# Kernel optimization log

Hardware: AMD Instinct MI355X
Metric: run time of the kernel (lower is better)

Reference implementation:

```python
import jax, jax.numpy as jnp
import numpy as np


def setup_inputs() -> dict:
    key = jax.random.key(0)
    k1, k2, k3 = jax.random.split(key, 3)
    B, D = 4096, 512
    out_ftir = jax.random.normal(k1, (B, D), dtype=jnp.float32)
    out_raman = jax.random.normal(k2, (B, D), dtype=jnp.float32)
    labels = jax.random.randint(k3, (B,), 0, 1000, dtype=jnp.int64)
    # learned parameter: log_tau = log(1/init_tau), init_tau = 0.07
    log_tau = jnp.asarray(np.log(1.0 / 0.07), dtype=jnp.float32)
    return {"out_ftir": out_ftir, "out_raman": out_raman, "labels": labels, "log_tau": log_tau}


def reference(out_ftir, out_raman, labels, log_tau):
    # temperature scale, clamped above at 100
    tau = jnp.minimum(jnp.exp(log_tau), 100.0)
    # [B, B] similarity logits
    logits = (out_ftir @ out_raman.T) * tau
    # CLIP-style symmetric cross-entropy with diagonal targets (arange(B)).
    # Note: original torch code's loop over positive off-diagonal pairs
    # computes an unused tensor and does not affect the output.
    raman_lp = jnp.diagonal(jax.nn.log_softmax(logits, axis=-1))   # rows: ftir -> raman
    ftir_lp = jnp.diagonal(jax.nn.log_softmax(logits.T, axis=-1))  # cols: raman -> ftir
    raman_loss = -jnp.mean(raman_lp)
    ftir_loss = -jnp.mean(ftir_lp)
    return (ftir_loss + raman_loss) / 2.0
```

## Files before the change

kernel.cpp:

```cpp
#include <hip/hip_runtime.h>
#include <hip/hip_bf16.h>
#include <stdint.h>


typedef float f32x4 __attribute__((ext_vector_type(4)));
typedef __bf16 bf16x8 __attribute__((ext_vector_type(8)));
typedef __bf16 bf16x4 __attribute__((ext_vector_type(4)));

#define B_DIM 4096
#define D_DIM 512
#define NCHUNK 32

__device__ __forceinline__ void gld_lds16(const void* g, void* l) {
  __builtin_amdgcn_global_load_lds(
      (const __attribute__((address_space(1))) unsigned int*)g,
      (__attribute__((address_space(3))) unsigned int*)l,
      16, 0, 0);
}

__global__ __launch_bounds__(256) void cast_diag_kernel(
    const float* __restrict__ A, const float* __restrict__ Bm,
    __bf16* __restrict__ Abf, __bf16* __restrict__ Bbf,
    float* __restrict__ diagp, float* __restrict__ acc,
    unsigned* __restrict__ counter) {
  if (blockIdx.x == 0 && threadIdx.x == 0) { acc[0] = 0.f; counter[0] = 0u; }
  const float4* A4 = (const float4*)A;
  const float4* B4 = (const float4*)Bm;
  bf16x4* Ab4 = (bf16x4*)Abf;
  bf16x4* Bb4 = (bf16x4*)Bbf;
  int idx = blockIdx.x * 256 + threadIdx.x;
  float local = 0.f;
  #pragma unroll
  for (int it = 0; it < 4; ++it, idx += 512 * 256) {
    int row = idx >> 7, el4 = idx & 127;
    int g = (el4 >> 1) & 3;
    int gswz = g ^ ((row >> 1) & 3);
    int el4p = (el4 & ~6) | (gswz << 1);
    int pidx = row * 128 + el4p;
    float4 va = A4[idx], vb = B4[idx];
    bf16x4 oa, ob;
    oa[0] = (__bf16)va.x; oa[1] = (__bf16)va.y; oa[2] = (__bf16)va.z; oa[3] = (__bf16)va.w;
    ob[0] = (__bf16)vb.x; ob[1] = (__bf16)vb.y; ob[2] = (__bf16)vb.z; ob[3] = (__bf16)vb.w;
    Ab4[pidx] = oa; Bb4[pidx] = ob;
    local += va.x*vb.x + va.y*vb.y + va.z*vb.z + va.w*vb.w;
  }
  #pragma unroll
  for (int off = 1; off < 64; off <<= 1) local += __shfl_xor(local, off);
  __shared__ float red[4];
  int w = threadIdx.x >> 6, lane = threadIdx.x & 63;
  if (lane == 0) red[w] = local;
  __syncthreads();
  if (threadIdx.x == 0)
    diagp[blockIdx.x] = red[0] + red[1] + red[2] + red[3];
}

__global__ __launch_bounds__(256, 3) void gemm_lse_kernel(
    const __bf16* __restrict__ A, const __bf16* __restrict__ Bm,
    const float* __restrict__ log_tau,
    float* __restrict__ row_pmax, float* __restrict__ row_psum,
    float* __restrict__ col_pmax, float* __restrict__ col_psum) {
  __shared__ char smem[49152];
  const int blk = blockIdx.x;
  const int xcd = blk & 7, loc = blk >> 3;
  const int bm = (xcd & 3) * 8 + (loc & 7);
  const int bn = (xcd >> 2) * 16 + (loc >> 3);
  const int t = threadIdx.x;
  const int lane = t & 63;
  const int w = t >> 6;
  const int wm = (w >> 1) * 64, wn = (w & 1) * 64;
  const int q = lane >> 4, c16 = lane & 15;
  const int kbs = q ^ ((c16 >> 1) & 3);

  f32x4 acc[4][4] = {};

  const char* Ag = (const char*)A + (size_t)(bm * 128 + (t >> 2)) * 1024 + (t & 3) * 16;
  const char* Bg = (const char*)Bm + (size_t)(bn * 128 + (t >> 2)) * 1024 + (t & 3) * 16;

  #define ISSUE_STAGE(kt, p)                                                  \
    do {                                                                      \
      const char* ag = Ag + (kt) * 64;                                        \
      const char* bg = Bg + (kt) * 64;                                        \
      char* Al = smem + (p) * 16384 + t * 16;                                 \
      char* Bl = smem + (p) * 16384 + 8192 + t * 16;                          \
      _Pragma("unroll")                                                       \
      for (int i = 0; i < 2; ++i) {                                           \
        gld_lds16(ag + i * 65536, Al + i * 4096);                             \
        gld_lds16(bg + i * 65536, Bl + i * 4096);                             \
      }                                                                       \
    } while (0)

  #define COMPUTE(p)                                                          \
    do {                                                                      \
      const char* Ab = smem + (p) * 16384;                                    \
      const char* Bb = Ab + 8192;                                             \
      bf16x8 af[4], bfr[4];                                                   \
      _Pragma("unroll")                                                       \
      for (int mi = 0; mi < 4; ++mi)                                          \
        af[mi] = *(const bf16x8*)(Ab + (wm + mi * 16 + c16) * 64 + kbs * 16); \
      _Pragma("unroll")                                                       \
      for (int ni = 0; ni < 4; ++ni)                                          \
        bfr[ni] = *(const bf16x8*)(Bb + (wn + ni * 16 + c16) * 64 + kbs * 16);\
      _Pragma("unroll")                                                       \
      for (int mi = 0; mi < 4; ++mi)                                          \
        _Pragma("unroll")                                                     \
        for (int ni = 0; ni < 4; ++ni)                                        \
          acc[mi][ni] = __builtin_amdgcn_mfma_f32_16x16x32_bf16(              \
              af[mi], bfr[ni], acc[mi][ni], 0, 0, 0);                         \
    } while (0)

  ISSUE_STAGE(0, 0);
  ISSUE_STAGE(1, 1);
  for (int kt = 0; kt < 15; ++kt) {
    asm volatile("s_waitcnt vmcnt(4)" ::: "memory");
    __builtin_amdgcn_s_barrier();
    asm volatile("" ::: "memory");
    if (kt < 14) ISSUE_STAGE(kt + 2, (kt + 2) % 3);
    COMPUTE(kt % 3);
  }
  asm volatile("s_waitcnt vmcnt(0)" ::: "memory");
  __builtin_amdgcn_s_barrier();
  asm volatile("" ::: "memory");
  COMPUTE(15 % 3);
  __syncthreads();
  #undef ISSUE_STAGE
  #undef COMPUTE

  const float tau = fminf(__expf(log_tau[0]), 100.0f);
  #pragma unroll
  for (int mi = 0; mi < 4; ++mi)
    #pragma unroll
    for (int ni = 0; ni < 4; ++ni)
      acc[mi][ni] *= tau;

  float2* rbuf = (float2*)smem;
  #pragma unroll
  for (int mi = 0; mi < 4; ++mi)
    #pragma unroll
    for (int r = 0; r < 4; ++r) {
      float v0 = acc[mi][0][r], v1 = acc[mi][1][r], v2 = acc[mi][2][r], v3 = acc[mi][3][r];
      float m = fmaxf(fmaxf(v0, v1), fmaxf(v2, v3));
      float s = __expf(v0 - m) + __expf(v1 - m) + __expf(v2 - m) + __expf(v3 - m);
      int R = wm + mi * 16 + q * 4 + r;
      rbuf[R * 33 + (w & 1) * 16 + c16] = make_float2(m, s);
    }
  __syncthreads();
  if (t < 128) {
    float M = rbuf[t * 33].x;
    #pragma unroll
    for (int x = 1; x < 32; ++x) M = fmaxf(M, rbuf[t * 33 + x].x);
    float S = 0.f;
    #pragma unroll
    for (int x = 0; x < 32; ++x) { float2 p = rbuf[t * 33 + x]; S += p.y * __expf(p.x - M); }
    row_pmax[bn * B_DIM + bm * 128 + t] = M;
    row_psum[bn * B_DIM + bm * 128 + t] = S;
  }
  __syncthreads();
  float2* cbuf = (float2*)smem;
  #pragma unroll
  for (int ni = 0; ni < 4; ++ni) {
    float m = -3.0e38f;
    #pragma unroll
    for (int mi = 0; mi < 4; ++mi)
      #pragma unroll
      for (int r = 0; r < 4; ++r) m = fmaxf(m, acc[mi][ni][r]);
    float s = 0.f;
    #pragma unroll
    for (int mi = 0; mi < 4; ++mi)
      #pragma unroll
      for (int r = 0; r < 4; ++r) s += __expf(acc[mi][ni][r] - m);
    int C = wn + ni * 16 + c16;
    cbuf[C * 9 + (w >> 1) * 4 + q] = make_float2(m, s);
  }
  __syncthreads();
  if (t < 128) {
    float M = cbuf[t * 9].x;
    #pragma unroll
    for (int y = 1; y < 8; ++y) M = fmaxf(M, cbuf[t * 9 + y].x);
    float S = 0.f;
    #pragma unroll
    for (int y = 0; y < 8; ++y) { float2 p = cbuf[t * 9 + y]; S += p.y * __expf(p.x - M); }
    col_pmax[bm * B_DIM + bn * 128 + t] = M;
    col_psum[bm * B_DIM + bn * 128 + t] = S;
  }
}

__global__ __launch_bounds__(256) void combine_kernel(
    const float* __restrict__ row_pmax, const float* __restrict__ row_psum,
    const float* __restrict__ col_pmax, const float* __restrict__ col_psum,
    const float* __restrict__ diagp, const float* __restrict__ log_tau,
    float* __restrict__ acc, unsigned* __restrict__ counter,
    float* __restrict__ out) {
  const int t = threadIdx.x;
  const int item = blockIdx.x * 256 + t;
  const float* pm; const float* ps; int i;
  if (item < B_DIM) { pm = row_pmax; ps = row_psum; i = item; }
  else              { pm = col_pmax; ps = col_psum; i = item - B_DIM; }
  float M = pm[i];
  #pragma unroll
  for (int k = 1; k < NCHUNK; ++k) M = fmaxf(M, pm[k * B_DIM + i]);
  float S = 0.f;
  #pragma unroll
  for (int k = 0; k < NCHUNK; ++k) S += ps[k * B_DIM + i] * __expf(pm[k * B_DIM + i] - M);
  float local = M + __logf(S);
  if (blockIdx.x == 0) {
    float tau = fminf(__expf(log_tau[0]), 100.0f);
    local += -2.0f * tau * (diagp[t] + diagp[t + 256]);
  }
  #pragma unroll
  for (int off = 1; off < 64; off <<= 1) local += __shfl_xor(local, off);
  __shared__ float red[4];
  int w = t >> 6, lane = t & 63;
  if (lane == 0) red[w] = local;
  __syncthreads();
  if (t == 0) {
    atomicAdd(acc, red[0] + red[1] + red[2] + red[3]);
    __threadfence();
    unsigned old = atomicAdd(counter, 1u);
    if (old == 31u) {
      float v = atomicAdd(acc, 0.0f);
      out[0] = v * (1.0f / 8192.0f);
    }
  }
}

extern "C" void kernel_launch(void* const* d_in, const int* in_sizes, int n_in,
                              void* d_out, int out_size, void* d_ws, size_t ws_size,
                              hipStream_t stream) {
  const float* ftir    = (const float*)d_in[0];
  const float* raman   = (const float*)d_in[1];
  const float* log_tau = (const float*)d_in[3];
  float* out = (float*)d_out;

  char* ws = (char*)d_ws;
  __bf16* Abf     = (__bf16*)(ws);
  __bf16* Bbf     = (__bf16*)(ws + (4u << 20));
  float* row_pmax = (float*)(ws + (8u << 20));
  float* row_psum = (float*)(ws + (8u << 20) + (512u << 10));
  float* col_pmax = (float*)(ws + (9u << 20));
  float* col_psum = (float*)(ws + (9u << 20) + (512u << 10));
  float* diagp    = (float*)(ws + (10u << 20));
  float* acc      = (float*)(ws + (10u << 20) + 4096);
  unsigned* cnt   = (unsigned*)(ws + (10u << 20) + 4096 + 4);

  cast_diag_kernel<<<512, 256, 0, stream>>>(ftir, raman, Abf, Bbf, diagp, acc, cnt);
  gemm_lse_kernel<<<1024, 256, 0, stream>>>(Abf, Bbf, log_tau,
                                            row_pmax, row_psum, col_pmax, col_psum);
  combine_kernel<<<32, 256, 0, stream>>>(row_pmax, row_psum, col_pmax, col_psum,
                                         diagp, log_tau, acc, cnt, out);
}
```

Measured before the change: 96.82 us.

## Fuse fp32-to-bf16 cast and diagonal into GEMM via register-staged loads

Removes the separate cast/diagonal kernel. The GEMM now loads fp32 inputs straight into registers, converts them to bf16 and writes swizzled tiles to LDS in a two-stage register-prefetch pipeline, in place of the earlier three-stage direct global-to-LDS async loads. The diagonal term is taken from the MFMA accumulators of the diagonal tiles and added atomically. This saves one launch and the bf16 round trip through global memory, but the GEMM now reads twice as many bytes and does the conversion in its main loop with a shallower pipeline, and the diagonal now comes from bf16 products rather than fp32.

```diff
diff --git a/kernel.cpp b/kernel.cpp
--- a/kernel.cpp
+++ b/kernel.cpp
@@ -5,61 +5,18 @@
 
 typedef float f32x4 __attribute__((ext_vector_type(4)));
 typedef __bf16 bf16x8 __attribute__((ext_vector_type(8)));
-typedef __bf16 bf16x4 __attribute__((ext_vector_type(4)));
 
 #define B_DIM 4096
 #define D_DIM 512
 #define NCHUNK 32
 
-__device__ __forceinline__ void gld_lds16(const void* g, void* l) {
-  __builtin_amdgcn_global_load_lds(
-      (const __attribute__((address_space(1))) unsigned int*)g,
-      (__attribute__((address_space(3))) unsigned int*)l,
-      16, 0, 0);
-}
-
-__global__ __launch_bounds__(256) void cast_diag_kernel(
-    const float* __restrict__ A, const float* __restrict__ Bm,
-    __bf16* __restrict__ Abf, __bf16* __restrict__ Bbf,
-    float* __restrict__ diagp, float* __restrict__ acc,
-    unsigned* __restrict__ counter) {
-  if (blockIdx.x == 0 && threadIdx.x == 0) { acc[0] = 0.f; counter[0] = 0u; }
-  const float4* A4 = (const float4*)A;
-  const float4* B4 = (const float4*)Bm;
-  bf16x4* Ab4 = (bf16x4*)Abf;
-  bf16x4* Bb4 = (bf16x4*)Bbf;
-  int idx = blockIdx.x * 256 + threadIdx.x;
-  float local = 0.f;
-  #pragma unroll
-  for (int it = 0; it < 4; ++it, idx += 512 * 256) {
-    int row = idx >> 7, el4 = idx & 127;
-    int g = (el4 >> 1) & 3;
-    int gswz = g ^ ((row >> 1) & 3);
-    int el4p = (el4 & ~6) | (gswz << 1);
-    int pidx = row * 128 + el4p;
-    float4 va = A4[idx], vb = B4[idx];
-    bf16x4 oa, ob;
-    oa[0] = (__bf16)va.x; oa[1] = (__bf16)va.y; oa[2] = (__bf16)va.z; oa[3] = (__bf16)va.w;
-    ob[0] = (__bf16)vb.x; ob[1] = (__bf16)vb.y; ob[2] = (__bf16)vb.z; ob[3] = (__bf16)vb.w;
-    Ab4[pidx] = oa; Bb4[pidx] = ob;
-    local += va.x*vb.x + va.y*vb.y + va.z*vb.z + va.w*vb.w;
-  }
-  #pragma unroll
-  for (int off = 1; off < 64; off <<= 1) local += __shfl_xor(local, off);
-  __shared__ float red[4];
-  int w = threadIdx.x >> 6, lane = threadIdx.x & 63;
-  if (lane == 0) red[w] = local;
-  __syncthreads();
-  if (threadIdx.x == 0)
-    diagp[blockIdx.x] = red[0] + red[1] + red[2] + red[3];
-}
-
 __global__ __launch_bounds__(256, 3) void gemm_lse_kernel(
-    const __bf16* __restrict__ A, const __bf16* __restrict__ Bm,
+    const float* __restrict__ Af, const float* __restrict__ Bf,
     const float* __restrict__ log_tau,
     float* __restrict__ row_pmax, float* __restrict__ row_psum,
-    float* __restrict__ col_pmax, float* __restrict__ col_psum) {
-  __shared__ char smem[49152];
+    float* __restrict__ col_pmax, float* __restrict__ col_psum,
+    float* __restrict__ accg) {
+  __shared__ char smem[34816];
   const int blk = blockIdx.x;
   const int xcd = blk & 7, loc = blk >> 3;
   const int bm = (xcd & 3) * 8 + (loc & 7);
@@ -73,20 +30,39 @@
 
   f32x4 acc[4][4] = {};
 
-  const char* Ag = (const char*)A + (size_t)(bm * 128 + (t >> 2)) * 1024 + (t & 3) * 16;
-  const char* Bg = (const char*)Bm + (size_t)(bn * 128 + (t >> 2)) * 1024 + (t & 3) * 16;
-
-  #define ISSUE_STAGE(kt, p)                                                  \
+  const int srow = t >> 1;
+  const int sw   = (t >> 2) & 3;
+  const int kb0  = (t & 1) * 2;
+  const float4* Ag0 = (const float4*)(Af + (size_t)(bm * 128 + srow) * D_DIM) + (t & 1) * 4;
+  const float4* Bg0 = (const float4*)(Bf + (size_t)(bn * 128 + srow) * D_DIM) + (t & 1) * 4;
+  const int ldsA = srow * 64 ;
+
+  float4 a0, a1, a2, a3, b0, b1, b2, b3;
+
+  #define LOADS(kt)                                                           \
     do {                                                                      \
-      const char* ag = Ag + (kt) * 64;                                        \
-      const char* bg = Bg + (kt) * 64;                                        \
-      char* Al = smem + (p) * 16384 + t * 16;                                 \
-      char* Bl = smem + (p) * 16384 + 8192 + t * 16;                          \
-      _Pragma("unroll")                                                       \
-      for (int i = 0; i < 2; ++i) {                                           \
-        gld_lds16(ag + i * 65536, Al + i * 4096);                             \
-        gld_lds16(bg + i * 65536, Bl + i * 4096);                             \
-      }                                                                       \
+      const float4* ag = Ag0 + (kt) * 8;                                      \
+      const float4* bg = Bg0 + (kt) * 8;                                      \
+      a0 = ag[0]; a1 = ag[1]; a2 = ag[2]; a3 = ag[3];                         \
+      b0 = bg[0]; b1 = bg[1]; b2 = bg[2]; b3 = bg[3];                         \
+    } while (0)
+
+  #define COMMIT(p)                                                           \
+    do {                                                                      \
+      bf16x8 pa0, pa1, pb0, pb1;                                              \
+      pa0[0]=(__bf16)a0.x; pa0[1]=(__bf16)a0.y; pa0[2]=(__bf16)a0.z; pa0[3]=(__bf16)a0.w; \
+      pa0[4]=(__bf16)a1.x; pa0[5]=(__bf16)a1.y; pa0[6]=(__bf16)a1.z; pa0[7]=(__bf16)a1.w; \
+      pa1[0]=(__bf16)a2.x; pa1[1]=(__bf16)a2.y; pa1[2]=(__bf16)a2.z; pa1[3]=(__bf16)a2.w; \
+      pa1[4]=(__bf16)a3.x; pa1[5]=(__bf16)a3.y; pa1[6]=(__bf16)a3.z; pa1[7]=(__bf16)a3.w; \
+      pb0[0]=(__bf16)b0.x; pb0[1]=(__bf16)b0.y; pb0[2]=(__bf16)b0.z; pb0[3]=(__bf16)b0.w; \
+      pb0[4]=(__bf16)b1.x; pb0[5]=(__bf16)b1.y; pb0[6]=(__bf16)b1.z; pb0[7]=(__bf16)b1.w; \
+      pb1[0]=(__bf16)b2.x; pb1[1]=(__bf16)b2.y; pb1[2]=(__bf16)b2.z; pb1[3]=(__bf16)b2.w; \
+      pb1[4]=(__bf16)b3.x; pb1[5]=(__bf16)b3.y; pb1[6]=(__bf16)b3.z; pb1[7]=(__bf16)b3.w; \
+      char* base = smem + (p) * 16384;                                        \
+      *(bf16x8*)(base + ldsA + ((kb0 ^ sw)) * 16)        = pa0;               \
+      *(bf16x8*)(base + ldsA + (((kb0 + 1) ^ sw)) * 16)  = pa1;               \
+      *(bf16x8*)(base + 8192 + ldsA + ((kb0 ^ sw)) * 16)       = pb0;         \
+      *(bf16x8*)(base + 8192 + ldsA + (((kb0 + 1) ^ sw)) * 16) = pb1;         \
     } while (0)
 
   #define COMPUTE(p)                                                          \
@@ -108,21 +84,17 @@
               af[mi], bfr[ni], acc[mi][ni], 0, 0, 0);                         \
     } while (0)
 
-  ISSUE_STAGE(0, 0);
-  ISSUE_STAGE(1, 1);
-  for (int kt = 0; kt < 15; ++kt) {
-    asm volatile("s_waitcnt vmcnt(4)" ::: "memory");
-    __builtin_amdgcn_s_barrier();
-    asm volatile("" ::: "memory");
-    if (kt < 14) ISSUE_STAGE(kt + 2, (kt + 2) % 3);
-    COMPUTE(kt % 3);
-  }
-  asm volatile("s_waitcnt vmcnt(0)" ::: "memory");
-  __builtin_amdgcn_s_barrier();
-  asm volatile("" ::: "memory");
-  COMPUTE(15 % 3);
-  __syncthreads();
-  #undef ISSUE_STAGE
+  LOADS(0);
+  COMMIT(0);
+  for (int kt = 0; kt < 16; ++kt) {
+    __syncthreads();
+    if (kt < 15) LOADS(kt + 1);
+    COMPUTE(kt & 1);
+    if (kt < 15) COMMIT((kt + 1) & 1);
+  }
+  __syncthreads();
+  #undef LOADS
+  #undef COMMIT
   #undef COMPUTE
 
   const float tau = fminf(__expf(log_tau[0]), 100.0f);
@@ -131,6 +103,20 @@
     #pragma unroll
     for (int ni = 0; ni < 4; ++ni)
       acc[mi][ni] *= tau;
+
+  if (bm == bn && (w == 0 || w == 3)) {
+    float dsum = 0.f;
+    int r = c16 - (q << 2);
+    #pragma unroll
+    for (int rr = 0; rr < 4; ++rr)
+      if (rr == r) {
+        #pragma unroll
+        for (int mi = 0; mi < 4; ++mi) dsum += acc[mi][mi][rr];
+      }
+    #pragma unroll
+    for (int off = 1; off < 64; off <<= 1) dsum += __shfl_xor(dsum, off);
+    if (lane == 0) atomicAdd(accg, -2.0f * dsum);
+  }
 
   float2* rbuf = (float2*)smem;
   #pragma unroll
@@ -187,7 +173,6 @@
 __global__ __launch_bounds__(256) void combine_kernel(
     const float* __restrict__ row_pmax, const float* __restrict__ row_psum,
     const float* __restrict__ col_pmax, const float* __restrict__ col_psum,
-    const float* __restrict__ diagp, const float* __restrict__ log_tau,
     float* __restrict__ acc, unsigned* __restrict__ counter,
     float* __restrict__ out) {
   const int t = threadIdx.x;
@@ -202,10 +187,6 @@
   #pragma unroll
   for (int k = 0; k < NCHUNK; ++k) S += ps[k * B_DIM + i] * __expf(pm[k * B_DIM + i] - M);
   float local = M + __logf(S);
-  if (blockIdx.x == 0) {
-    float tau = fminf(__expf(log_tau[0]), 100.0f);
-    local += -2.0f * tau * (diagp[t] + diagp[t + 256]);
-  }
   #pragma unroll
   for (int off = 1; off < 64; off <<= 1) local += __shfl_xor(local, off);
   __shared__ float red[4];
@@ -232,19 +213,16 @@
   float* out = (float*)d_out;
 
   char* ws = (char*)d_ws;
-  __bf16* Abf     = (__bf16*)(ws);
-  __bf16* Bbf     = (__bf16*)(ws + (4u << 20));
-  float* row_pmax = (float*)(ws + (8u << 20));
-  float* row_psum = (float*)(ws + (8u << 20) + (512u << 10));
-  float* col_pmax = (float*)(ws + (9u << 20));
-  float* col_psum = (float*)(ws + (9u << 20) + (512u << 10));
-  float* diagp    = (float*)(ws + (10u << 20));
-  float* acc      = (float*)(ws + (10u << 20) + 4096);
-  unsigned* cnt   = (unsigned*)(ws + (10u << 20) + 4096 + 4);
-
-  cast_diag_kernel<<<512, 256, 0, stream>>>(ftir, raman, Abf, Bbf, diagp, acc, cnt);
-  gemm_lse_kernel<<<1024, 256, 0, stream>>>(Abf, Bbf, log_tau,
-                                            row_pmax, row_psum, col_pmax, col_psum);
+  float* row_pmax = (float*)(ws);
+  float* row_psum = (float*)(ws + (512u << 10));
+  float* col_pmax = (float*)(ws + (1024u << 10));
+  float* col_psum = (float*)(ws + (1536u << 10));
+  float* acc      = (float*)(ws + (2048u << 10));
+  unsigned* cnt   = (unsigned*)(ws + (2048u << 10) + 4);
+
+  hipMemsetAsync(acc, 0, 8, stream);
+  gemm_lse_kernel<<<1024, 256, 0, stream>>>(ftir, raman, log_tau,
+                                            row_pmax, row_psum, col_pmax, col_psum, acc);
   combine_kernel<<<32, 256, 0, stream>>>(row_pmax, row_psum, col_pmax, col_psum,
-                                         diagp, log_tau, acc, cnt, out);
+                                         acc, cnt, out);
 }
```

After: 120.4 us. +24.4%, slower.

## Fuse bf16 cast and diagonal pass into GEMM kernel with per-panel readiness flags

Applied to the files above, without the earlier changes.

Merges the cast and diagonal kernel into the GEMM-LSE kernel. Blocks first pull cast work slices from per-XCD atomic queues, then spin on per-panel counters until their A and B row panels are converted before starting the GEMM. This removes a kernel launch boundary and lets the GEMM start on ready panels while other panels are still being cast. In exchange it adds atomics, spin-waiting and a memset, and relies on forward progress of the resident blocks.

```diff
diff --git a/kernel.cpp b/kernel.cpp
--- a/kernel.cpp
+++ b/kernel.cpp
@@ -18,45 +18,13 @@
       16, 0, 0);
 }
 
-__global__ __launch_bounds__(256) void cast_diag_kernel(
-    const float* __restrict__ A, const float* __restrict__ Bm,
+__global__ __launch_bounds__(256, 3) void fused_kernel(
+    const float* __restrict__ Af, const float* __restrict__ Bf,
+    const float* __restrict__ log_tau,
     __bf16* __restrict__ Abf, __bf16* __restrict__ Bbf,
-    float* __restrict__ diagp, float* __restrict__ acc,
-    unsigned* __restrict__ counter) {
-  if (blockIdx.x == 0 && threadIdx.x == 0) { acc[0] = 0.f; counter[0] = 0u; }
-  const float4* A4 = (const float4*)A;
-  const float4* B4 = (const float4*)Bm;
-  bf16x4* Ab4 = (bf16x4*)Abf;
-  bf16x4* Bb4 = (bf16x4*)Bbf;
-  int idx = blockIdx.x * 256 + threadIdx.x;
-  float local = 0.f;
-  #pragma unroll
-  for (int it = 0; it < 4; ++it, idx += 512 * 256) {
-    int row = idx >> 7, el4 = idx & 127;
-    int g = (el4 >> 1) & 3;
-    int gswz = g ^ ((row >> 1) & 3);
-    int el4p = (el4 & ~6) | (gswz << 1);
-    int pidx = row * 128 + el4p;
-    float4 va = A4[idx], vb = B4[idx];
-    bf16x4 oa, ob;
-    oa[0] = (__bf16)va.x; oa[1] = (__bf16)va.y; oa[2] = (__bf16)va.z; oa[3] = (__bf16)va.w;
-    ob[0] = (__bf16)vb.x; ob[1] = (__bf16)vb.y; ob[2] = (__bf16)vb.z; ob[3] = (__bf16)vb.w;
-    Ab4[pidx] = oa; Bb4[pidx] = ob;
-    local += va.x*vb.x + va.y*vb.y + va.z*vb.z + va.w*vb.w;
-  }
-  #pragma unroll
-  for (int off = 1; off < 64; off <<= 1) local += __shfl_xor(local, off);
-  __shared__ float red[4];
-  int w = threadIdx.x >> 6, lane = threadIdx.x & 63;
-  if (lane == 0) red[w] = local;
-  __syncthreads();
-  if (threadIdx.x == 0)
-    diagp[blockIdx.x] = red[0] + red[1] + red[2] + red[3];
-}
-
-__global__ __launch_bounds__(256, 3) void gemm_lse_kernel(
-    const __bf16* __restrict__ A, const __bf16* __restrict__ Bm,
-    const float* __restrict__ log_tau,
+    float* __restrict__ diagp,
+    unsigned* __restrict__ qcnt,
+    unsigned* __restrict__ pcnt,
     float* __restrict__ row_pmax, float* __restrict__ row_psum,
     float* __restrict__ col_pmax, float* __restrict__ col_psum) {
   __shared__ char smem[49152];
@@ -67,14 +35,64 @@
   const int t = threadIdx.x;
   const int lane = t & 63;
   const int w = t >> 6;
+
+  volatile int* sh_i = (volatile int*)smem;
+  volatile float* sh_f = (volatile float*)(smem + 64);
+  const float4* A4 = (const float4*)Af;
+  const float4* B4 = (const float4*)Bf;
+  bf16x4* Ab4 = (bf16x4*)Abf;
+  bf16x4* Bb4 = (bf16x4*)Bbf;
+  for (;;) {
+    __syncthreads();
+    if (t == 0) sh_i[0] = (int)atomicAdd(&qcnt[xcd], 1u);
+    __syncthreads();
+    int sl = sh_i[0];
+    if (sl >= 64) break;
+    int s = xcd * 64 + sl;
+    float local = 0.f;
+    #pragma unroll
+    for (int it = 0; it < 4; ++it) {
+      int idx = s * 1024 + it * 256 + t;
+      int row = idx >> 7, el4 = idx & 127;
+      int g = (el4 >> 1) & 3;
+      int gswz = g ^ ((row >> 1) & 3);
+      int el4p = (el4 & ~6) | (gswz << 1);
+      int pidx = row * 128 + el4p;
+      float4 va = A4[idx], vb = B4[idx];
+      bf16x4 oa, ob;
+      oa[0]=(__bf16)va.x; oa[1]=(__bf16)va.y; oa[2]=(__bf16)va.z; oa[3]=(__bf16)va.w;
+      ob[0]=(__bf16)vb.x; ob[1]=(__bf16)vb.y; ob[2]=(__bf16)vb.z; ob[3]=(__bf16)vb.w;
+      Ab4[pidx] = oa; Bb4[pidx] = ob;
+      local += va.x*vb.x + va.y*vb.y + va.z*vb.z + va.w*vb.w;
+    }
+    #pragma unroll
+    for (int off = 1; off < 64; off <<= 1) local += __shfl_xor(local, off);
+    if (lane == 0) sh_f[w] = local;
+    __syncthreads();
+    if (t == 0) {
+      diagp[s] = sh_f[0] + sh_f[1] + sh_f[2] + sh_f[3];
+      __threadfence();
+      atomicAdd(&pcnt[s >> 4], 1u);
+    }
+  }
+
+  if (t == 0) {
+    while (__hip_atomic_load(&pcnt[bm], __ATOMIC_RELAXED, __HIP_MEMORY_SCOPE_AGENT) < 16u)
+      __builtin_amdgcn_s_sleep(16);
+    while (__hip_atomic_load(&pcnt[bn], __ATOMIC_RELAXED, __HIP_MEMORY_SCOPE_AGENT) < 16u)
+      __builtin_amdgcn_s_sleep(16);
+  }
+  __syncthreads();
+  __threadfence();
+
   const int wm = (w >> 1) * 64, wn = (w & 1) * 64;
   const int q = lane >> 4, c16 = lane & 15;
   const int kbs = q ^ ((c16 >> 1) & 3);
 
   f32x4 acc[4][4] = {};
 
-  const char* Ag = (const char*)A + (size_t)(bm * 128 + (t >> 2)) * 1024 + (t & 3) * 16;
-  const char* Bg = (const char*)Bm + (size_t)(bn * 128 + (t >> 2)) * 1024 + (t & 3) * 16;
+  const char* Ag = (const char*)Abf + (size_t)(bm * 128 + (t >> 2)) * 1024 + (t & 3) * 16;
+  const char* Bg = (const char*)Bbf + (size_t)(bn * 128 + (t >> 2)) * 1024 + (t & 3) * 16;
 
   #define ISSUE_STAGE(kt, p)                                                  \
     do {                                                                      \
@@ -108,6 +126,7 @@
               af[mi], bfr[ni], acc[mi][ni], 0, 0, 0);                         \
     } while (0)
 
+  __syncthreads();
   ISSUE_STAGE(0, 0);
   ISSUE_STAGE(1, 1);
   for (int kt = 0; kt < 15; ++kt) {
@@ -239,12 +258,16 @@
   float* col_pmax = (float*)(ws + (9u << 20));
   float* col_psum = (float*)(ws + (9u << 20) + (512u << 10));
   float* diagp    = (float*)(ws + (10u << 20));
-  float* acc      = (float*)(ws + (10u << 20) + 4096);
-  unsigned* cnt   = (unsigned*)(ws + (10u << 20) + 4096 + 4);
-
-  cast_diag_kernel<<<512, 256, 0, stream>>>(ftir, raman, Abf, Bbf, diagp, acc, cnt);
-  gemm_lse_kernel<<<1024, 256, 0, stream>>>(Abf, Bbf, log_tau,
-                                            row_pmax, row_psum, col_pmax, col_psum);
+  char*  flags    = ws + (10u << 20) + 4096;
+  float*    acc   = (float*)(flags);
+  unsigned* cnt   = (unsigned*)(flags + 4);
+  unsigned* qcnt  = (unsigned*)(flags + 8);
+  unsigned* pcnt  = (unsigned*)(flags + 8 + 32);
+
+  hipMemsetAsync(flags, 0, 8 + 32 + 128, stream);
+  fused_kernel<<<1024, 256, 0, stream>>>(ftir, raman, log_tau, Abf, Bbf, diagp,
+                                         qcnt, pcnt,
+                                         row_pmax, row_psum, col_pmax, col_psum);
   combine_kernel<<<32, 256, 0, stream>>>(row_pmax, row_psum, col_pmax, col_psum,
                                          diagp, log_tau, acc, cnt, out);
 }
```

Measured after the change: 238.3 us. 2.46x slower.

## Fuse final LSE combine into GEMM kernel via per-stripe completion counters

Applied to the files above, without the earlier changes.

Removes the separate combine kernel launch. Each GEMM block increments counters for its row stripe and column stripe, and the last block to finish a stripe does the 32-way log-sum-exp merge for those 128 rows or columns plus the diagonal term, then adds into a global accumulator. A final counter decides which block writes the output. This saves one kernel launch and its dependency gap, at the cost of extra atomics, fences and a serialized tail reduction in a few GEMM blocks.

```diff
diff --git a/kernel.cpp b/kernel.cpp
--- a/kernel.cpp
+++ b/kernel.cpp
@@ -9,7 +9,6 @@
 
 #define B_DIM 4096
 #define D_DIM 512
-#define NCHUNK 32
 
 __device__ __forceinline__ void gld_lds16(const void* g, void* l) {
   __builtin_amdgcn_global_load_lds(
@@ -21,9 +20,8 @@
 __global__ __launch_bounds__(256) void cast_diag_kernel(
     const float* __restrict__ A, const float* __restrict__ Bm,
     __bf16* __restrict__ Abf, __bf16* __restrict__ Bbf,
-    float* __restrict__ diagp, float* __restrict__ acc,
-    unsigned* __restrict__ counter) {
-  if (blockIdx.x == 0 && threadIdx.x == 0) { acc[0] = 0.f; counter[0] = 0u; }
+    float* __restrict__ diagp, unsigned* __restrict__ flags) {
+  if (blockIdx.x == 0 && threadIdx.x < 66) flags[threadIdx.x] = 0u;
   const float4* A4 = (const float4*)A;
   const float4* B4 = (const float4*)Bm;
   bf16x4* Ab4 = (bf16x4*)Abf;
@@ -39,8 +37,8 @@
     int pidx = row * 128 + el4p;
     float4 va = A4[idx], vb = B4[idx];
     bf16x4 oa, ob;
-    oa[0] = (__bf16)va.x; oa[1] = (__bf16)va.y; oa[2] = (__bf16)va.z; oa[3] = (__bf16)va.w;
-    ob[0] = (__bf16)vb.x; ob[1] = (__bf16)vb.y; ob[2] = (__bf16)vb.z; ob[3] = (__bf16)vb.w;
+    oa[0]=(__bf16)va.x; oa[1]=(__bf16)va.y; oa[2]=(__bf16)va.z; oa[3]=(__bf16)va.w;
+    ob[0]=(__bf16)vb.x; ob[1]=(__bf16)vb.y; ob[2]=(__bf16)vb.z; ob[3]=(__bf16)vb.w;
     Ab4[pidx] = oa; Bb4[pidx] = ob;
     local += va.x*vb.x + va.y*vb.y + va.z*vb.z + va.w*vb.w;
   }
@@ -56,10 +54,17 @@
 
 __global__ __launch_bounds__(256, 3) void gemm_lse_kernel(
     const __bf16* __restrict__ A, const __bf16* __restrict__ Bm,
-    const float* __restrict__ log_tau,
+    const float* __restrict__ log_tau, const float* __restrict__ diagp,
     float* __restrict__ row_pmax, float* __restrict__ row_psum,
-    float* __restrict__ col_pmax, float* __restrict__ col_psum) {
+    float* __restrict__ col_pmax, float* __restrict__ col_psum,
+    unsigned* __restrict__ flags, float* __restrict__ out) {
   __shared__ char smem[49152];
+  __shared__ unsigned sflag;
+  __shared__ float red2[4];
+  float* acc            = (float*)flags;
+  unsigned* finish      = flags + 1;
+  unsigned* rowdone     = flags + 2;
+  unsigned* coldone     = flags + 34;
   const int blk = blockIdx.x;
   const int xcd = blk & 7, loc = blk >> 3;
   const int bm = (xcd & 3) * 8 + (loc & 7);
@@ -71,7 +76,7 @@
   const int q = lane >> 4, c16 = lane & 15;
   const int kbs = q ^ ((c16 >> 1) & 3);
 
-  f32x4 acc[4][4] = {};
+  f32x4 acc_r[4][4] = {};
 
   const char* Ag = (const char*)A + (size_t)(bm * 128 + (t >> 2)) * 1024 + (t & 3) * 16;
   const char* Bg = (const char*)Bm + (size_t)(bn * 128 + (t >> 2)) * 1024 + (t & 3) * 16;
@@ -104,8 +109,8 @@
       for (int mi = 0; mi < 4; ++mi)                                          \
         _Pragma("unroll")                                                     \
         for (int ni = 0; ni < 4; ++ni)                                        \
-          acc[mi][ni] = __builtin_amdgcn_mfma_f32_16x16x32_bf16(              \
-              af[mi], bfr[ni], acc[mi][ni], 0, 0, 0);                         \
+          acc_r[mi][ni] = __builtin_amdgcn_mfma_f32_16x16x32_bf16(            \
+              af[mi], bfr[ni], acc_r[mi][ni], 0, 0, 0);                       \
     } while (0)
 
   ISSUE_STAGE(0, 0);
@@ -130,14 +135,14 @@
   for (int mi = 0; mi < 4; ++mi)
     #pragma unroll
     for (int ni = 0; ni < 4; ++ni)
-      acc[mi][ni] *= tau;
+      acc_r[mi][ni] *= tau;
 
   float2* rbuf = (float2*)smem;
   #pragma unroll
   for (int mi = 0; mi < 4; ++mi)
     #pragma unroll
     for (int r = 0; r < 4; ++r) {
-      float v0 = acc[mi][0][r], v1 = acc[mi][1][r], v2 = acc[mi][2][r], v3 = acc[mi][3][r];
+      float v0 = acc_r[mi][0][r], v1 = acc_r[mi][1][r], v2 = acc_r[mi][2][r], v3 = acc_r[mi][3][r];
       float m = fmaxf(fmaxf(v0, v1), fmaxf(v2, v3));
       float s = __expf(v0 - m) + __expf(v1 - m) + __expf(v2 - m) + __expf(v3 - m);
       int R = wm + mi * 16 + q * 4 + r;
@@ -162,12 +167,12 @@
     #pragma unroll
     for (int mi = 0; mi < 4; ++mi)
       #pragma unroll
-      for (int r = 0; r < 4; ++r) m = fmaxf(m, acc[mi][ni][r]);
+      for (int r = 0; r < 4; ++r) m = fmaxf(m, acc_r[mi][ni][r]);
     float s = 0.f;
     #pragma unroll
     for (int mi = 0; mi < 4; ++mi)
       #pragma unroll
-      for (int r = 0; r < 4; ++r) s += __expf(acc[mi][ni][r] - m);
+      for (int r = 0; r < 4; ++r) s += __expf(acc_r[mi][ni][r] - m);
     int C = wn + ni * 16 + c16;
     cbuf[C * 9 + (w >> 1) * 4 + q] = make_float2(m, s);
   }
@@ -182,43 +187,69 @@
     col_pmax[bm * B_DIM + bn * 128 + t] = M;
     col_psum[bm * B_DIM + bn * 128 + t] = S;
   }
-}
-
-__global__ __launch_bounds__(256) void combine_kernel(
-    const float* __restrict__ row_pmax, const float* __restrict__ row_psum,
-    const float* __restrict__ col_pmax, const float* __restrict__ col_psum,
-    const float* __restrict__ diagp, const float* __restrict__ log_tau,
-    float* __restrict__ acc, unsigned* __restrict__ counter,
-    float* __restrict__ out) {
-  const int t = threadIdx.x;
-  const int item = blockIdx.x * 256 + t;
-  const float* pm; const float* ps; int i;
-  if (item < B_DIM) { pm = row_pmax; ps = row_psum; i = item; }
-  else              { pm = col_pmax; ps = col_psum; i = item - B_DIM; }
-  float M = pm[i];
-  #pragma unroll
-  for (int k = 1; k < NCHUNK; ++k) M = fmaxf(M, pm[k * B_DIM + i]);
-  float S = 0.f;
-  #pragma unroll
-  for (int k = 0; k < NCHUNK; ++k) S += ps[k * B_DIM + i] * __expf(pm[k * B_DIM + i] - M);
-  float local = M + __logf(S);
-  if (blockIdx.x == 0) {
-    float tau = fminf(__expf(log_tau[0]), 100.0f);
-    local += -2.0f * tau * (diagp[t] + diagp[t + 256]);
-  }
-  #pragma unroll
-  for (int off = 1; off < 64; off <<= 1) local += __shfl_xor(local, off);
-  __shared__ float red[4];
-  int w = t >> 6, lane = t & 63;
-  if (lane == 0) red[w] = local;
+
   __syncthreads();
   if (t == 0) {
-    atomicAdd(acc, red[0] + red[1] + red[2] + red[3]);
     __threadfence();
-    unsigned old = atomicAdd(counter, 1u);
-    if (old == 31u) {
-      float v = atomicAdd(acc, 0.0f);
-      out[0] = v * (1.0f / 8192.0f);
+    unsigned r1 = atomicAdd(&rowdone[bm], 1u);
+    unsigned r2 = atomicAdd(&coldone[bn], 1u);
+    sflag = (r1 == 31u ? 1u : 0u) | (r2 == 31u ? 2u : 0u);
+  }
+  __syncthreads();
+  const unsigned f = sflag;
+  if (f != 0u) {
+    __threadfence();
+    float tot = 0.f;
+    if (f & 1u) {
+      float local = 0.f;
+      if (t < 128) {
+        const int item = bm * 128 + t;
+        float M = row_pmax[item];
+        #pragma unroll
+        for (int k = 1; k < 32; ++k) M = fmaxf(M, row_pmax[k * B_DIM + item]);
+        float S = 0.f;
+        #pragma unroll
+        for (int k = 0; k < 32; ++k)
+          S += row_psum[k * B_DIM + item] * __expf(row_pmax[k * B_DIM + item] - M);
+        local = M + __logf(S);
+      } else if (t < 144) {
+        local = -2.0f * tau * diagp[bm * 16 + (t - 128)];
+      }
+      #pragma unroll
+      for (int off = 1; off < 64; off <<= 1) local += __shfl_xor(local, off);
+      if (lane == 0) red2[w] = local;
+      __syncthreads();
+      if (t == 0) tot += red2[0] + red2[1] + red2[2] + red2[3];
+      __syncthreads();
+    }
+    if (f & 2u) {
+      float local = 0.f;
+      if (t < 128) {
+        const int item = bn * 128 + t;
+        float M = col_pmax[item];
+        #pragma unroll
+        for (int k = 1; k < 32; ++k) M = fmaxf(M, col_pmax[k * B_DIM + item]);
+        float S = 0.f;
+        #pragma unroll
+        for (int k = 0; k < 32; ++k)
+          S += col_psum[k * B_DIM + item] * __expf(col_pmax[k * B_DIM + item] - M);
+        local = M + __logf(S);
+      }
+      #pragma unroll
+      for (int off = 1; off < 64; off <<= 1) local += __shfl_xor(local, off);
+      if (lane == 0) red2[w] = local;
+      __syncthreads();
+      if (t == 0) tot += red2[0] + red2[1] + red2[2] + red2[3];
+    }
+    if (t == 0) {
+      atomicAdd(acc, tot);
+      __threadfence();
+      const unsigned n = (f == 3u) ? 2u : 1u;
+      unsigned old = atomicAdd(finish, n);
+      if (old + n == 64u) {
+        float v = atomicAdd(acc, 0.0f);
+        out[0] = v * (1.0f / 8192.0f);
+      }
     }
   }
 }
@@ -239,12 +270,10 @@
   float* col_pmax = (float*)(ws + (9u << 20));
   float* col_psum = (float*)(ws + (9u << 20) + (512u << 10));
   float* diagp    = (float*)(ws + (10u << 20));
-  float* acc      = (float*)(ws + (10u << 20) + 4096);
-  unsigned* cnt   = (unsigned*)(ws + (10u << 20) + 4096 + 4);
-
-  cast_diag_kernel<<<512, 256, 0, stream>>>(ftir, raman, Abf, Bbf, diagp, acc, cnt);
-  gemm_lse_kernel<<<1024, 256, 0, stream>>>(Abf, Bbf, log_tau,
-                                            row_pmax, row_psum, col_pmax, col_psum);
-  combine_kernel<<<32, 256, 0, stream>>>(row_pmax, row_psum, col_pmax, col_psum,
-                                         diagp, log_tau, acc, cnt, out);
-}
+  unsigned* flags = (unsigned*)(ws + (10u << 20) + 4096);
+
+  cast_diag_kernel<<<512, 256, 0, stream>>>(ftir, raman, Abf, Bbf, diagp, flags);
+  gemm_lse_kernel<<<1024, 256, 0, stream>>>(Abf, Bbf, log_tau, diagp,
+                                            row_pmax, row_psum, col_pmax, col_psum,
+                                            flags, out);
+}
```

New measurement: 143.4 us. +48.1%, slower.
